# Kernel optimization log

Hardware: AMD Instinct MI355X
Metric: run time of the kernel (lower is better)

The kernel has to match this reference:

```python
import jax, jax.numpy as jnp
import numpy as np

NY, NX = 4096, 4096
VP = 3.1415 / 6.0  # particle volume, d=1
DX = 1.0
DY = 1.0


def setup_inputs() -> dict:
    key = jax.random.key(0)
    k1, k2, k3, k4, k5, k6, k7 = jax.random.split(key, 7)
    shape = (1, 1, NY, NX)
    # Eulerian node coordinates (meshgrid)
    xs = jnp.arange(NX, dtype=jnp.float32)
    ys = jnp.arange(NY, dtype=jnp.float32)
    x_grid = jnp.broadcast_to(xs[None, None, None, :], shape)
    y_grid = jnp.broadcast_to(ys[None, None, :, None], shape)
    # Lagrangian particle positions: node coordinate + sub-cell offset
    xp_grid = x_grid + jax.random.uniform(k1, shape, jnp.float32, -0.5, 0.5)
    yp_grid = y_grid + jax.random.uniform(k2, shape, jnp.float32, -0.5, 0.5)
    vx_grid = jax.random.normal(k3, shape, jnp.float32)
    vy_grid = jax.random.normal(k4, shape, jnp.float32)
    Fx_grid = jax.random.normal(k5, shape, jnp.float32)
    Fy_grid = jax.random.normal(k6, shape, jnp.float32)
    mask = (jax.random.uniform(k7, shape, jnp.float32) < 0.3).astype(jnp.float32)
    return {"xp_grid": xp_grid, "yp_grid": yp_grid, "x_grid": x_grid,
            "y_grid": y_grid, "vx_grid": vx_grid, "vy_grid": vy_grid,
            "Fx_grid": Fx_grid, "Fy_grid": Fy_grid, "mask": mask}


def reference(xp_grid, yp_grid, x_grid, y_grid, vx_grid, vy_grid, Fx_grid, Fy_grid, mask):
    # coupling_backward: interpolate particle quantities to Eulerian nodes
    # via a 3x3 linear-spline stencil of torch.roll-shifted fields.
    dt = xp_grid.dtype
    zero = jnp.zeros_like(xp_grid)
    alpha = zero
    alpha_u = zero
    alpha_v = zero
    Fx = zero
    Fy = zero
    inv_area = 1.0 / (DX * DY)
    for i in range(3):
        for j in range(3):
            sh = (j - 1, i - 1)
            sgn_x = jnp.roll(xp_grid, sh, axis=(2, 3)) - x_grid
            sgn_y = jnp.roll(yp_grid, sh, axis=(2, 3)) - y_grid
            Sx = jnp.where(sgn_x >= 0, jnp.float32(1.0), jnp.float32(-1.0)).astype(dt)
            Sy = jnp.where(sgn_y >= 0, jnp.float32(1.0), jnp.float32(-1.0)).astype(dt)
            xii = (2.0 * sgn_x - Sx * DX) / DX
            phi = (2.0 * sgn_y - Sy * DY) / DY
            in_x = ((xii >= -1.0) & (xii <= 1.0)).astype(dt)
            in_y = ((phi >= -1.0) & (phi <= 1.0)).astype(dt)
            N_xii = 0.5 * (1.0 - Sx * xii) * in_x
            N_phi = 0.5 * (1.0 - Sy * phi) * in_y
            w = N_xii * N_phi * mask * VP * inv_area  # per-tap spline weight
            alpha = alpha + w
            alpha_u = alpha_u + w * jnp.roll(vx_grid, sh, axis=(2, 3))
            alpha_v = alpha_v + w * jnp.roll(vy_grid, sh, axis=(2, 3))
            Fx = Fx + w * jnp.roll(Fx_grid, sh, axis=(2, 3))
            Fy = Fy + w * jnp.roll(Fy_grid, sh, axis=(2, 3))
    return jnp.stack([alpha, alpha_u, alpha_v, Fx, Fy])
```

## Files before the change

### kernel.cpp

```cpp
#include <hip/hip_runtime.h>


typedef float v4f __attribute__((ext_vector_type(4)));

static constexpr int NXd = 4096;
static constexpr int NYd = 4096;

__device__ __forceinline__ float hat(float s) {
    return fmaxf(1.0f - fabsf(s), 0.0f);
}

__device__ __forceinline__ void load_window6(const float* __restrict__ base,
                                             int voff, int voffl, int voffr,
                                             float w[6]) {
    v4f v = *reinterpret_cast<const v4f*>(base + voff);
    w[0] = base[voffl];
    w[1] = v[0]; w[2] = v[1]; w[3] = v[2]; w[4] = v[3];
    w[5] = base[voffr];
}

__global__ __launch_bounds__(256) void ai4dem_kernel(
    const float* __restrict__ xp, const float* __restrict__ yp,
    const float* __restrict__ vx, const float* __restrict__ vy,
    const float* __restrict__ fxg, const float* __restrict__ fyg,
    const float* __restrict__ mask, float* __restrict__ out)
{
    const int tx = threadIdx.x;
    const int ty = threadIdx.y;
    const int x0 = (blockIdx.x * 64 + tx) * 4;
    const int y  = blockIdx.y * 4 + ty;

    const int xl = (x0 == 0)       ? (NXd - 1) : (x0 - 1);
    const int xr = (x0 + 4 >= NXd) ? 0         : (x0 + 4);
    const float yf  = (float)y;
    const float xf0 = (float)x0;

    float accA[4] = {0.f,0.f,0.f,0.f};
    float accU[4] = {0.f,0.f,0.f,0.f};
    float accV[4] = {0.f,0.f,0.f,0.f};
    float accX[4] = {0.f,0.f,0.f,0.f};
    float accY[4] = {0.f,0.f,0.f,0.f};

    #pragma unroll
    for (int dy = -1; dy <= 1; ++dy) {
        int yy = y + dy;
        yy = (yy < 0) ? (NYd - 1) : ((yy >= NYd) ? 0 : yy);
        const int rb    = yy * NXd;
        const int voff  = rb + x0;
        const int voffl = rb + xl;
        const int voffr = rb + xr;

        float wxp[6], wyp[6];
        load_window6(xp, voff, voffl, voffr, wxp);
        load_window6(yp, voff, voffl, voffr, wyp);

        #pragma unroll
        for (int i = 0; i < 6; ++i) wyp[i] = hat(wyp[i] - yf);

        float w[12];
        #pragma unroll
        for (int k = 0; k < 4; ++k)
            #pragma unroll
            for (int c = 0; c < 3; ++c)
                w[k*3 + c] = hat(wxp[k + c] - (xf0 + (float)k)) * wyp[k + c];

        #pragma unroll
        for (int k = 0; k < 4; ++k)
            accA[k] += (w[k*3] + w[k*3+1]) + w[k*3+2];

        float win[6];
        load_window6(vx, voff, voffl, voffr, win);
        #pragma unroll
        for (int k = 0; k < 4; ++k)
            accU[k] = fmaf(w[k*3+2], win[k+2],
                      fmaf(w[k*3+1], win[k+1],
                      fmaf(w[k*3+0], win[k+0], accU[k])));

        load_window6(vy, voff, voffl, voffr, win);
        #pragma unroll
        for (int k = 0; k < 4; ++k)
            accV[k] = fmaf(w[k*3+2], win[k+2],
                      fmaf(w[k*3+1], win[k+1],
                      fmaf(w[k*3+0], win[k+0], accV[k])));

        load_window6(fxg, voff, voffl, voffr, win);
        #pragma unroll
        for (int k = 0; k < 4; ++k)
            accX[k] = fmaf(w[k*3+2], win[k+2],
                      fmaf(w[k*3+1], win[k+1],
                      fmaf(w[k*3+0], win[k+0], accX[k])));

        load_window6(fyg, voff, voffl, voffr, win);
        #pragma unroll
        for (int k = 0; k < 4; ++k)
            accY[k] = fmaf(w[k*3+2], win[k+2],
                      fmaf(w[k*3+1], win[k+1],
                      fmaf(w[k*3+0], win[k+0], accY[k])));
    }

    const float VPf = (float)(3.1415 / 6.0);
    const size_t ob    = (size_t)y * NXd + x0;
    const size_t plane = (size_t)NXd * NYd;

    v4f mv = *reinterpret_cast<const v4f*>(mask + ob);
    float m[4] = { mv[0] * VPf, mv[1] * VPf, mv[2] * VPf, mv[3] * VPf };

    v4f o;
    o[0] = accA[0]*m[0]; o[1] = accA[1]*m[1]; o[2] = accA[2]*m[2]; o[3] = accA[3]*m[3];
    __builtin_nontemporal_store(o, reinterpret_cast<v4f*>(out + ob));

    o[0] = accU[0]*m[0]; o[1] = accU[1]*m[1]; o[2] = accU[2]*m[2]; o[3] = accU[3]*m[3];
    __builtin_nontemporal_store(o, reinterpret_cast<v4f*>(out + plane + ob));

    o[0] = accV[0]*m[0]; o[1] = accV[1]*m[1]; o[2] = accV[2]*m[2]; o[3] = accV[3]*m[3];
    __builtin_nontemporal_store(o, reinterpret_cast<v4f*>(out + 2*plane + ob));

    o[0] = accX[0]*m[0]; o[1] = accX[1]*m[1]; o[2] = accX[2]*m[2]; o[3] = accX[3]*m[3];
    __builtin_nontemporal_store(o, reinterpret_cast<v4f*>(out + 3*plane + ob));

    o[0] = accY[0]*m[0]; o[1] = accY[1]*m[1]; o[2] = accY[2]*m[2]; o[3] = accY[3]*m[3];
    __builtin_nontemporal_store(o, reinterpret_cast<v4f*>(out + 4*plane + ob));
}

extern "C" void kernel_launch(void* const* d_in, const int* in_sizes, int n_in,
                              void* d_out, int out_size, void* d_ws, size_t ws_size,
                              hipStream_t stream) {
    const float* xp   = (const float*)d_in[0];
    const float* yp   = (const float*)d_in[1];
    const float* vx   = (const float*)d_in[4];
    const float* vy   = (const float*)d_in[5];
    const float* fxg  = (const float*)d_in[6];
    const float* fyg  = (const float*)d_in[7];
    const float* mask = (const float*)d_in[8];
    float* out = (float*)d_out;

    dim3 block(64, 4, 1);
    dim3 grid(NXd / 256, NYd / 4, 1);
    hipLaunchKernelGGL(ai4dem_kernel, grid, block, 0, stream,
                       xp, yp, vx, vy, fxg, fyg, mask, out);
}
```

Baseline: 731.7 us.

## Sweep rows per thread with rotating accumulators to load each input row once

Each thread now walks a column strip of 16 output rows. It loads each input row window once and scatters its contribution into three rotating accumulator sets for output rows y-1, y and y+1, writing out a row once its third contribution is in. Before, every input row was loaded three times by neighbouring output rows. This removes that redundant global and L2 traffic, costing a 2-row halo per strip, more live registers and fewer blocks (1024 blocks of 256 threads).

```diff
diff --git a/kernel.cpp b/kernel.cpp
--- a/kernel.cpp
+++ b/kernel.cpp
@@ -5,6 +5,7 @@
 
 static constexpr int NXd = 4096;
 static constexpr int NYd = 4096;
+static constexpr int H   = 16;
 
 __device__ __forceinline__ float hat(float s) {
     return fmaxf(1.0f - fabsf(s), 0.0f);
@@ -19,6 +20,86 @@
     w[5] = base[voffr];
 }
 
+struct Acc { float a[4], u[4], v[4], x[4], y[4]; };
+
+__device__ __forceinline__ void zero_acc(Acc& A) {
+    #pragma unroll
+    for (int k = 0; k < 4; ++k) { A.a[k]=0.f; A.u[k]=0.f; A.v[k]=0.f; A.x[k]=0.f; A.y[k]=0.f; }
+}
+
+__device__ __forceinline__ void accum(Acc& A, const float nx[12], const float wyp[6],
+                                      float yof,
+                                      const float wvx[6], const float wvy[6],
+                                      const float wfx[6], const float wfy[6]) {
+    float ny[6];
+    #pragma unroll
+    for (int i = 0; i < 6; ++i) ny[i] = hat(wyp[i] - yof);
+    #pragma unroll
+    for (int k = 0; k < 4; ++k) {
+        const float w0 = nx[k*3+0] * ny[k+0];
+        const float w1 = nx[k*3+1] * ny[k+1];
+        const float w2 = nx[k*3+2] * ny[k+2];
+        A.a[k] += (w0 + w1) + w2;
+        A.u[k] = fmaf(w2, wvx[k+2], fmaf(w1, wvx[k+1], fmaf(w0, wvx[k+0], A.u[k])));
+        A.v[k] = fmaf(w2, wvy[k+2], fmaf(w1, wvy[k+1], fmaf(w0, wvy[k+0], A.v[k])));
+        A.x[k] = fmaf(w2, wfx[k+2], fmaf(w1, wfx[k+1], fmaf(w0, wfx[k+0], A.x[k])));
+        A.y[k] = fmaf(w2, wfy[k+2], fmaf(w1, wfy[k+1], fmaf(w0, wfy[k+0], A.y[k])));
+    }
+}
+
+__device__ __forceinline__ void retire(const Acc& A, v4f mv, int o, int x0,
+                                       float* __restrict__ out) {
+    const float VPf = (float)(3.1415 / 6.0);
+    const size_t ob    = (size_t)o * NXd + x0;
+    const size_t plane = (size_t)NXd * NYd;
+    float m[4] = { mv[0]*VPf, mv[1]*VPf, mv[2]*VPf, mv[3]*VPf };
+    v4f t;
+    t[0]=A.a[0]*m[0]; t[1]=A.a[1]*m[1]; t[2]=A.a[2]*m[2]; t[3]=A.a[3]*m[3];
+    __builtin_nontemporal_store(t, reinterpret_cast<v4f*>(out + ob));
+    t[0]=A.u[0]*m[0]; t[1]=A.u[1]*m[1]; t[2]=A.u[2]*m[2]; t[3]=A.u[3]*m[3];
+    __builtin_nontemporal_store(t, reinterpret_cast<v4f*>(out + plane + ob));
+    t[0]=A.v[0]*m[0]; t[1]=A.v[1]*m[1]; t[2]=A.v[2]*m[2]; t[3]=A.v[3]*m[3];
+    __builtin_nontemporal_store(t, reinterpret_cast<v4f*>(out + 2*plane + ob));
+    t[0]=A.x[0]*m[0]; t[1]=A.x[1]*m[1]; t[2]=A.x[2]*m[2]; t[3]=A.x[3]*m[3];
+    __builtin_nontemporal_store(t, reinterpret_cast<v4f*>(out + 3*plane + ob));
+    t[0]=A.y[0]*m[0]; t[1]=A.y[1]*m[1]; t[2]=A.y[2]*m[2]; t[3]=A.y[3]*m[3];
+    __builtin_nontemporal_store(t, reinterpret_cast<v4f*>(out + 4*plane + ob));
+}
+
+#define STEP(T, AM1, A0, AP1)                                                  \
+  {                                                                            \
+    const int t  = (T);                                                        \
+    const int yu = ys - 1 + t;                       \
+    const int yy = (yu < 0) ? (NYd - 1) : ((yu >= NYd) ? 0 : yu);              \
+    const int rb = yy * NXd;                                                   \
+    const int voff  = rb + x0;                                                 \
+    const int voffl = rb + xl;                                                 \
+    const int voffr = rb + xr;                                                 \
+    const bool live = (t >= 2);                     \
+    v4f mv{};                                                                  \
+    if (live) mv = *reinterpret_cast<const v4f*>(mask + (size_t)(yu-1)*NXd + x0); \
+    float wxp[6], wyp[6], wvx[6], wvy[6], wfx[6], wfy[6];                      \
+    load_window6(xp,  voff, voffl, voffr, wxp);                                \
+    load_window6(yp,  voff, voffl, voffr, wyp);                                \
+    load_window6(vx,  voff, voffl, voffr, wvx);                                \
+    load_window6(vy,  voff, voffl, voffr, wvy);                                \
+    load_window6(fxg, voff, voffl, voffr, wfx);                                \
+    load_window6(fyg, voff, voffl, voffr, wfy);                                \
+    float nx[12];                                                              \
+    _Pragma("unroll")                                                          \
+    for (int k = 0; k < 4; ++k) {                                              \
+      _Pragma("unroll")                                                        \
+      for (int c = 0; c < 3; ++c)                                              \
+        nx[k*3+c] = hat(wxp[k+c] - (xf0 + (float)k));                          \
+    }                                                                          \
+    const float yuf = (float)yu;                                               \
+    accum(AM1, nx, wyp, yuf - 1.0f, wvx, wvy, wfx, wfy);                       \
+    accum(A0,  nx, wyp, yuf,        wvx, wvy, wfx, wfy);                       \
+    accum(AP1, nx, wyp, yuf + 1.0f, wvx, wvy, wfx, wfy);                       \
+    if (live) retire(AM1, mv, yu - 1, x0, out);                                \
+    zero_acc(AM1);                                                             \
+  }
+
 __global__ __launch_bounds__(256) void ai4dem_kernel(
     const float* __restrict__ xp, const float* __restrict__ yp,
     const float* __restrict__ vx, const float* __restrict__ vy,
@@ -26,100 +107,23 @@
     const float* __restrict__ mask, float* __restrict__ out)
 {
     const int tx = threadIdx.x;
-    const int ty = threadIdx.y;
-    const int x0 = (blockIdx.x * 64 + tx) * 4;
-    const int y  = blockIdx.y * 4 + ty;
+    const int x0 = (blockIdx.x * 256 + tx) * 4;
+    const int ys = blockIdx.y * H;
 
     const int xl = (x0 == 0)       ? (NXd - 1) : (x0 - 1);
     const int xr = (x0 + 4 >= NXd) ? 0         : (x0 + 4);
-    const float yf  = (float)y;
     const float xf0 = (float)x0;
 
-    float accA[4] = {0.f,0.f,0.f,0.f};
-    float accU[4] = {0.f,0.f,0.f,0.f};
-    float accV[4] = {0.f,0.f,0.f,0.f};
-    float accX[4] = {0.f,0.f,0.f,0.f};
-    float accY[4] = {0.f,0.f,0.f,0.f};
+    Acc A, B, C;
+    zero_acc(A); zero_acc(B); zero_acc(C);
 
-    #pragma unroll
-    for (int dy = -1; dy <= 1; ++dy) {
-        int yy = y + dy;
-        yy = (yy < 0) ? (NYd - 1) : ((yy >= NYd) ? 0 : yy);
-        const int rb    = yy * NXd;
-        const int voff  = rb + x0;
-        const int voffl = rb + xl;
-        const int voffr = rb + xr;
-
-        float wxp[6], wyp[6];
-        load_window6(xp, voff, voffl, voffr, wxp);
-        load_window6(yp, voff, voffl, voffr, wyp);
-
-        #pragma unroll
-        for (int i = 0; i < 6; ++i) wyp[i] = hat(wyp[i] - yf);
-
-        float w[12];
-        #pragma unroll
-        for (int k = 0; k < 4; ++k)
-            #pragma unroll
-            for (int c = 0; c < 3; ++c)
-                w[k*3 + c] = hat(wxp[k + c] - (xf0 + (float)k)) * wyp[k + c];
-
-        #pragma unroll
-        for (int k = 0; k < 4; ++k)
-            accA[k] += (w[k*3] + w[k*3+1]) + w[k*3+2];
-
-        float win[6];
-        load_window6(vx, voff, voffl, voffr, win);
-        #pragma unroll
-        for (int k = 0; k < 4; ++k)
-            accU[k] = fmaf(w[k*3+2], win[k+2],
-                      fmaf(w[k*3+1], win[k+1],
-                      fmaf(w[k*3+0], win[k+0], accU[k])));
-
-        load_window6(vy, voff, voffl, voffr, win);
-        #pragma unroll
-        for (int k = 0; k < 4; ++k)
-            accV[k] = fmaf(w[k*3+2], win[k+2],
-                      fmaf(w[k*3+1], win[k+1],
-                      fmaf(w[k*3+0], win[k+0], accV[k])));
-
-        load_window6(fxg, voff, voffl, voffr, win);
-        #pragma unroll
-        for (int k = 0; k < 4; ++k)
-            accX[k] = fmaf(w[k*3+2], win[k+2],
-                      fmaf(w[k*3+1], win[k+1],
-                      fmaf(w[k*3+0], win[k+0], accX[k])));
-
-        load_window6(fyg, voff, voffl, voffr, win);
-        #pragma unroll
-        for (int k = 0; k < 4; ++k)
-            accY[k] = fmaf(w[k*3+2], win[k+2],
-                      fmaf(w[k*3+1], win[k+1],
-                      fmaf(w[k*3+0], win[k+0], accY[k])));
+    #pragma unroll 2
+    for (int it = 0; it < (H + 2) / 3; ++it) {
+        const int tb = it * 3;
+        STEP(tb + 0, A, B, C);
+        STEP(tb + 1, B, C, A);
+        STEP(tb + 2, C, A, B);
     }
-
-    const float VPf = (float)(3.1415 / 6.0);
-    const size_t ob    = (size_t)y * NXd + x0;
-    const size_t plane = (size_t)NXd * NYd;
-
-    v4f mv = *reinterpret_cast<const v4f*>(mask + ob);
-    float m[4] = { mv[0] * VPf, mv[1] * VPf, mv[2] * VPf, mv[3] * VPf };
-
-    v4f o;
-    o[0] = accA[0]*m[0]; o[1] = accA[1]*m[1]; o[2] = accA[2]*m[2]; o[3] = accA[3]*m[3];
-    __builtin_nontemporal_store(o, reinterpret_cast<v4f*>(out + ob));
-
-    o[0] = accU[0]*m[0]; o[1] = accU[1]*m[1]; o[2] = accU[2]*m[2]; o[3] = accU[3]*m[3];
-    __builtin_nontemporal_store(o, reinterpret_cast<v4f*>(out + plane + ob));
-
-    o[0] = accV[0]*m[0]; o[1] = accV[1]*m[1]; o[2] = accV[2]*m[2]; o[3] = accV[3]*m[3];
-    __builtin_nontemporal_store(o, reinterpret_cast<v4f*>(out + 2*plane + ob));
-
-    o[0] = accX[0]*m[0]; o[1] = accX[1]*m[1]; o[2] = accX[2]*m[2]; o[3] = accX[3]*m[3];
-    __builtin_nontemporal_store(o, reinterpret_cast<v4f*>(out + 3*plane + ob));
-
-    o[0] = accY[0]*m[0]; o[1] = accY[1]*m[1]; o[2] = accY[2]*m[2]; o[3] = accY[3]*m[3];
-    __builtin_nontemporal_store(o, reinterpret_cast<v4f*>(out + 4*plane + ob));
 }
 
 extern "C" void kernel_launch(void* const* d_in, const int* in_sizes, int n_in,
@@ -134,8 +138,8 @@
     const float* mask = (const float*)d_in[8];
     float* out = (float*)d_out;
 
-    dim3 block(64, 4, 1);
-    dim3 grid(NXd / 256, NYd / 4, 1);
+    dim3 block(256, 1, 1);
+    dim3 grid(NXd / 1024, NYd / H, 1);
     hipLaunchKernelGGL(ai4dem_kernel, grid, block, 0, stream,
                        xp, yp, vx, vy, fxg, fyg, mask, out);
 }
```

Result: no change. 718.2 us (-1.8%).
